# Kernel optimization log

Measured on AMD Instinct MI355X. Metric: run time of the kernel, lower is better.

The kernel has to match this reference:

```python
import jax, jax.numpy as jnp
import numpy as np

DN = ('NCHW', 'OIHW', 'NCHW')

def _conv(x, w, b):
    y = jax.lax.conv_general_dilated(x, w, (2, 2), 'SAME', dimension_numbers=DN)
    return jax.nn.relu(y + b[None, :, None, None])

def setup_inputs() -> dict:
    key = jax.random.key(0)
    ks = jax.random.split(key, 20)
    B, S, V, D, NC = 64, 128, 32000, 512, 1000
    inp = {}
    inp['images'] = jax.random.normal(ks[0], (B, 3, 224, 224), jnp.float32)
    inp['sequences'] = jax.random.randint(ks[1], (B, S), 0, V)
    inp['lengths'] = jax.random.randint(ks[2], (B,), 1, S + 1)
    inp['lengths_var'] = inp['lengths']
    s = 0.02
    inp['emb'] = jax.random.normal(ks[3], (V, D), jnp.float32) * s
    # SimpleCNN(3): 4 strided conv blocks 3->64->128->256->512, final_dim=512
    chans = [3, 64, 128, 256, 512]
    for i in range(4):
        inp[f'cw{i+1}'] = jax.random.normal(ks[4 + i], (chans[i + 1], chans[i], 3, 3), jnp.float32) * s
        inp[f'cb{i+1}'] = jnp.zeros((chans[i + 1],), jnp.float32)
    inp['rnn_w'] = jax.random.normal(ks[8], (D, D), jnp.float32) * s
    inp['rnn_b'] = jnp.zeros((D,), jnp.float32)
    inp['fc1_w'] = jax.random.normal(ks[9], (D + 512, 512), jnp.float32) * s
    inp['fc1_b'] = jnp.zeros((512,), jnp.float32)
    inp['fc2_w'] = jax.random.normal(ks[10], (512, 512), jnp.float32) * s
    inp['fc2_b'] = jnp.zeros((512,), jnp.float32)
    inp['clf_w'] = jax.random.normal(ks[11], (512, NC), jnp.float32) * s
    inp['clf_b'] = jnp.zeros((NC,), jnp.float32)
    return inp

def reference(images, sequences, lengths, lengths_var, emb, cw1, cb1, cw2, cb2, cw3, cb3, cw4, cb4, rnn_w, rnn_b, fc1_w, fc1_b, fc2_w, fc2_b, clf_w, clf_b):
    B, S = sequences.shape
    # masked mean over valid tokens (replaces the per-sample python loop)
    we = emb[sequences]                                   # [B,S,512]
    mask = (jnp.arange(S)[None, :] < lengths[:, None]).astype(we.dtype)
    batch_means = (we * mask[:, :, None]).sum(1) / lengths.astype(we.dtype)[:, None]
    sent = batch_means @ rnn_w + rnn_b                    # [B,512]
    # SimpleCNN + global avg pool -> [B,512,1,1] -> squeeze
    x = _conv(images, cw1, cb1)
    x = _conv(x, cw2, cb2)
    x = _conv(x, cw3, cb3)
    x = _conv(x, cw4, cb4)
    img = x.mean(axis=(2, 3))                             # [B,512]
    feats = jnp.concatenate([img, sent], axis=1)          # [B,1024]
    h = jax.nn.relu(feats @ fc1_w + fc1_b)
    h = jax.nn.relu(h @ fc2_w + fc2_b)                    # dropout = identity (eval)
    return h @ clf_w + clf_b
```

## Files before the change

### kernel.cpp

```cpp
#include <hip/hip_runtime.h>
#include <hip/hip_bf16.h>
#include <cstddef>
#include <cstdint>

typedef unsigned short u16;
typedef __attribute__((ext_vector_type(8))) short bf16x8;
typedef __attribute__((ext_vector_type(4))) float f32x4;
typedef __attribute__((ext_vector_type(8))) unsigned short u16x8;

static __device__ __forceinline__ u16 f2bf(float x) {
  unsigned u = __float_as_uint(x);
  u += 0x7fffu + ((u >> 16) & 1u);
  return (u16)(u >> 16);
}
static __device__ __forceinline__ float bflo(unsigned u) { return __uint_as_float(u << 16); }
static __device__ __forceinline__ float bfhi(unsigned u) { return __uint_as_float(u & 0xffff0000u); }

static __device__ __forceinline__ void gll16(const u16* g, u16* l) {
  __builtin_amdgcn_global_load_lds(
      (const __attribute__((address_space(1))) void*)g,
      (__attribute__((address_space(3))) void*)l, 16, 0, 0);
}

static __device__ __forceinline__ int xcd_swizzle(int orig, int nwg) {
  const int q = nwg >> 3, r = nwg & 7;
  const int xcd = orig & 7, idx = orig >> 3;
  return (xcd < r ? xcd * (q + 1) : r * (q + 1) + (xcd - r) * q) + idx;
}

static __device__ __forceinline__ void halo_store(u16* buf, int H, int W, int C,
                                                  long long i) {
  const int c8n = C >> 3;
  const int c8 = (int)(i % c8n);
  long long rem = i / c8n;
  const int p = (int)(rem % (W + 1 + H));
  const int n = (int)(rem / (W + 1 + H));
  int y, x;
  if (p <= W) { y = H; x = p; } else { y = p - (W + 1); x = W; }
  const u16x8 z = {0, 0, 0, 0, 0, 0, 0, 0};
  *(u16x8*)(buf + (((size_t)n * (H + 1) + y) * (W + 1) + x) * C + c8 * 8) = z;
}
__global__ __launch_bounds__(256) void zero_halo3(u16* __restrict__ A,
                                                  u16* __restrict__ B,
                                                  u16* __restrict__ Cb, int nimg) {
  long long i = (long long)blockIdx.x * 256 + threadIdx.x;
  const long long cA = (long long)nimg * 225 * 8;
  const long long cB = (long long)nimg * 113 * 16;
  const long long cC = (long long)nimg * 57 * 32;
  if (i < cA) { halo_store(A, 112, 112, 64, i); return; }
  i -= cA;
  if (i < cB) { halo_store(B, 56, 56, 128, i); return; }
  i -= cB;
  if (i < cC) halo_store(Cb, 28, 28, 256, i);
}

__global__ __launch_bounds__(256) void conv1_s2(
    const float* __restrict__ in,
    const float* __restrict__ w,
    const float* __restrict__ bias,
    u16* __restrict__ out) {
  __shared__ float sw[64 * 27];
  __shared__ float sb[64];
  __shared__ u16 so[256 * 64];
  const int tid = threadIdx.x;
  if (tid < 64) sb[tid] = bias[tid];
  for (int i = tid; i < 64 * 27; i += 256) sw[i] = w[i];
  __syncthreads();
  const int n = blockIdx.y;
  const int by = blockIdx.x / 7, bx = blockIdx.x % 7;
  const int oy = by * 16 + (tid >> 4), ox = bx * 16 + (tid & 15);
  const bool colv = (ox != 111);
  const float* ib = in + (size_t)n * 3 * 224 * 224 + (size_t)(2 * oy) * 224 + 2 * ox;

  float v[27];
  #pragma unroll
  for (int c = 0; c < 3; ++c)
    #pragma unroll
    for (int r = 0; r < 3; ++r) {
      const bool rowv = !(oy == 111 && r == 2);
      const float* rp = ib + (size_t)c * 50176 + r * 224;
      float2 p = {0.f, 0.f};
      float x2 = 0.f;
      if (rowv) {
        p = *(const float2*)rp;
        if (colv) x2 = rp[2];
      }
      v[c * 9 + r * 3 + 0] = p.x;
      v[c * 9 + r * 3 + 1] = p.y;
      v[c * 9 + r * 3 + 2] = x2;
    }

  #pragma unroll
  for (int kc = 0; kc < 8; ++kc) {
    u16x8 pack;
    #pragma unroll
    for (int k8 = 0; k8 < 8; ++k8) {
      const int k = kc * 8 + k8;
      float a = sb[k];
      const float* wk = &sw[k * 27];
      #pragma unroll
      for (int t = 0; t < 27; ++t) a = fmaf(v[t], wk[t], a);
      pack[k8] = f2bf(fmaxf(a, 0.f));
    }
    *(u16x8*)&so[(tid * 8 + (kc ^ (tid & 7))) * 8] = pack;
  }
  __syncthreads();
  u16* obase = out + (((size_t)n * 113 + by * 16) * 113 + bx * 16) * 64;
  #pragma unroll
  for (int it = 0; it < 8; ++it) {
    const int row = it * 2 + (tid >> 7);
    const int q = tid & 127;
    const int px = q >> 3, c8 = q & 7;
    const int p = row * 16 + px;
    u16x8 v8 = *(const u16x8*)&so[(p * 8 + (c8 ^ (p & 7))) * 8];
    *(u16x8*)(obase + ((size_t)row * 113 + px) * 64 + c8 * 8) = v8;
  }
}

static __device__ __forceinline__ void pack_one(const float* __restrict__ w,
                                                u16* __restrict__ pw,
                                                int CB, int NB, int C, int idx) {
  const int j = idx & 7;
  const int L = (idx >> 3) & 63;
  int t = idx >> 9;
  const int nbg = t % NB; t /= NB;
  const int cb = t % CB;
  const int tap = t / CB;
  const int n = nbg * 16 + (L & 15);
  const int c = cb * 32 + ((L >> 4) << 3) + j;
  pw[idx] = f2bf(w[((size_t)n * C + c) * 9 + tap]);
}
__global__ __launch_bounds__(256) void pack_all(
    const float* __restrict__ w2, const float* __restrict__ w3,
    const float* __restrict__ w4, u16* __restrict__ p2,
    u16* __restrict__ p3, u16* __restrict__ p4) {
  int i = blockIdx.x * 256 + threadIdx.x;
  if (i < 9 * 64 * 128) { pack_one(w2, p2, 2, 8, 64, i); return; }
  i -= 9 * 64 * 128;
  if (i < 9 * 128 * 256) { pack_one(w3, p3, 4, 16, 128, i); return; }
  i -= 9 * 128 * 256;
  if (i < 9 * 256 * 512) pack_one(w4, p4, 8, 32, 256, i);
}

template<int C, int K, int OH, int OW>
__global__ __launch_bounds__(256, 3) void conv3x3s2_mfma(
    const u16* __restrict__ in,
    const u16* __restrict__ pw,
    const float* __restrict__ bias,
    u16* __restrict__ out,
    int M_total) {
  constexpr int IH = 2 * OH, IW = 2 * OW;
  constexpr int PIW = IW + 1;
  constexpr int P = OH * OW;
  constexpr int CB = C / 32, NB = K / 16;
  constexpr int STEPS = 9 * CB;
  static_assert(STEPS % 3 == 0, "triple-buffer rotation needs STEPS%3==0");

  __shared__ u16 lds[3][8192];

  const int bm = xcd_swizzle(blockIdx.x, gridDim.x);
  const int nbh = blockIdx.y;
  const int lane = threadIdx.x & 63, wv = threadIdx.x >> 6;
  const int mh = wv >> 1, nh = wv & 1;

  int s_aoff[4];
  #pragma unroll
  for (int mf = 0; mf < 4; ++mf) {
    int pm = bm * 128 + mh * 64 + mf * 16 + (lane & 15);
    if (pm >= M_total) pm = M_total - 1;
    const int n = pm / P;
    const int p = pm - n * P;
    const int oy = p / OW, ox = p - oy * OW;
    s_aoff[mf] = ((n * (IH + 1) + 2 * oy) * PIW + 2 * ox) * C + ((lane >> 4) << 3);
  }

  f32x4 acc[4][4];
  #pragma unroll
  for (int mf = 0; mf < 4; ++mf)
    #pragma unroll
    for (int nf = 0; nf < 4; ++nf) acc[mf][nf] = (f32x4){0.f, 0.f, 0.f, 0.f};

  auto STAGE = [&](int st, int buf) {
    if (nh == 0) {
      const int cb = st & (CB - 1);
      const int tap = st / CB;
      const int r = tap / 3, s = tap - 3 * r;
      const int toff = (r * PIW + s) * C + cb * 32;
      #pragma unroll
      for (int mf = 0; mf < 4; ++mf)
        gll16(in + s_aoff[mf] + toff, &lds[buf][(mh * 4 + mf) * 512]);
    } else {
      const u16* bp = pw + ((size_t)st * NB + nbh * 8 + mh * 4) * 512 + lane * 8;
      #pragma unroll
      for (int nf = 0; nf < 4; ++nf)
        gll16(bp + nf * 512, &lds[buf][4096 + (mh * 4 + nf) * 512]);
    }
  };
  auto COMPUTE = [&](int buf) {
    bf16x8 a[4], b[4];
    #pragma unroll
    for (int mf = 0; mf < 4; ++mf)
      a[mf] = *(const bf16x8*)&lds[buf][(mh * 4 + mf) * 512 + lane * 8];
    #pragma unroll
    for (int nf = 0; nf < 4; ++nf)
      b[nf] = *(const bf16x8*)&lds[buf][4096 + (nh * 4 + nf) * 512 + lane * 8];
    #pragma unroll
    for (int mf = 0; mf < 4; ++mf)
      #pragma unroll
      for (int nf = 0; nf < 4; ++nf)
        acc[mf][nf] = __builtin_amdgcn_mfma_f32_16x16x32_bf16(a[mf], b[nf], acc[mf][nf], 0, 0, 0);
  };
  auto PHASE = [&](int s, int bufC, int bufS) {
    const bool more = (s + 2) < STEPS;
    if (more) STAGE(s + 2, bufS);
    __builtin_amdgcn_s_setprio(1);
    COMPUTE(bufC);
    __builtin_amdgcn_s_setprio(0);
    if (more) asm volatile("s_waitcnt vmcnt(4)" ::: "memory");
    else      asm volatile("s_waitcnt vmcnt(0)" ::: "memory");
    __builtin_amdgcn_s_barrier();
    __builtin_amdgcn_sched_barrier(0);
  };

  STAGE(0, 0);
  STAGE(1, 1);
  asm volatile("s_waitcnt vmcnt(4)" ::: "memory");
  __builtin_amdgcn_s_barrier();
  __builtin_amdgcn_sched_barrier(0);

  for (int st = 0; st < STEPS; st += 3) {
    PHASE(st + 0, 0, 2);
    PHASE(st + 1, 1, 0);
    PHASE(st + 2, 2, 1);
  }

  const int rowg = (lane >> 4) << 2;
  #pragma unroll
  for (int mf = 0; mf < 4; ++mf)
    #pragma unroll
    for (int nf = 0; nf < 4; ++nf) {
      const int ch = (nbh * 8 + nh * 4 + nf) * 16 + (lane & 15);
      const float bv = bias[ch];
      #pragma unroll
      for (int rr = 0; rr < 4; ++rr) {
        const int pm = bm * 128 + mh * 64 + mf * 16 + rowg + rr;
        if (pm < M_total) {
          const int n = pm / P;
          const int p = pm - n * P;
          const int oy = p / OW, ox = p - oy * OW;
          out[(((size_t)n * (OH + 1) + oy) * (OW + 1) + ox) * K + ch] =
              f2bf(fmaxf(acc[mf][nf][rr] + bv, 0.f));
        }
      }
    }
}

__global__ __launch_bounds__(256) void avgpool_nhwc(
    const u16* __restrict__ in, float* __restrict__ feats, int n0) {
  const int n = blockIdx.x, t = threadIdx.x;
  const u16* p = in + (size_t)n * (15 * 15 * 512) + t * 2;
  float s0 = 0.f, s1 = 0.f;
  for (int y = 0; y < 14; ++y)
    #pragma unroll
    for (int x = 0; x < 14; ++x) {
      unsigned u = *(const unsigned*)(p + (size_t)(y * 15 + x) * 512);
      s0 += bflo(u);
      s1 += bfhi(u);
    }
  float* f = feats + (size_t)(n0 + n) * 1024;
  f[2 * t] = s0 * (1.f / 196.f);
  f[2 * t + 1] = s1 * (1.f / 196.f);
}

__global__ __launch_bounds__(256) void embed_mean_kernel(
    const int* __restrict__ seq, const int* __restrict__ len,
    const float* __restrict__ emb, float* __restrict__ means) {
  __shared__ float part[3][512];
  const int b = blockIdx.x;
  const int L = len[b];
  const int sg = threadIdx.x >> 6;
  const int d0 = (threadIdx.x & 63) * 8;
  float a[8] = {0.f, 0.f, 0.f, 0.f, 0.f, 0.f, 0.f, 0.f};
  for (int s = sg; s < L; s += 4) {
    const float* e = emb + (size_t)seq[b * 128 + s] * 512 + d0;
    float4 v0 = *(const float4*)e, v1 = *(const float4*)(e + 4);
    a[0] += v0.x; a[1] += v0.y; a[2] += v0.z; a[3] += v0.w;
    a[4] += v1.x; a[5] += v1.y; a[6] += v1.z; a[7] += v1.w;
  }
  if (sg) {
    #pragma unroll
    for (int j = 0; j < 8; ++j) part[sg - 1][d0 + j] = a[j];
  }
  __syncthreads();
  if (sg == 0) {
    const float inv = 1.f / (float)L;
    #pragma unroll
    for (int j = 0; j < 8; ++j)
      means[(size_t)b * 512 + d0 + j] =
          (a[j] + part[0][d0 + j] + part[1][d0 + j] + part[2][d0 + j]) * inv;
  }
}

template<int K, int N, bool RELU>
__global__ __launch_bounds__(256) void fc_kernel(
    const float* __restrict__ x, int ldx,
    const float* __restrict__ w, const float* __restrict__ bias,
    float* __restrict__ out, int ldo) {
  __shared__ float row[2][K];
  const int m0 = blockIdx.y * 2;
  for (int i = threadIdx.x; i < 2 * K; i += 256)
    row[i / K][i % K] = x[(size_t)(m0 + i / K) * ldx + (i % K)];
  __syncthreads();
  const int col = blockIdx.x * 256 + threadIdx.x;
  if (col < N) {
    float acc[2][4] = {{0.f, 0.f, 0.f, 0.f}, {0.f, 0.f, 0.f, 0.f}};
    for (int k = 0; k < K; k += 4) {
      float w0 = w[(size_t)(k + 0) * N + col];
      float w1 = w[(size_t)(k + 1) * N + col];
      float w2 = w[(size_t)(k + 2) * N + col];
      float w3 = w[(size_t)(k + 3) * N + col];
      #pragma unroll
      for (int m = 0; m < 2; ++m) {
        acc[m][0] = fmaf(row[m][k + 0], w0, acc[m][0]);
        acc[m][1] = fmaf(row[m][k + 1], w1, acc[m][1]);
        acc[m][2] = fmaf(row[m][k + 2], w2, acc[m][2]);
        acc[m][3] = fmaf(row[m][k + 3], w3, acc[m][3]);
      }
    }
    const float bv = bias[col];
    #pragma unroll
    for (int m = 0; m < 2; ++m) {
      float a = acc[m][0] + acc[m][1] + acc[m][2] + acc[m][3] + bv;
      out[(size_t)(m0 + m) * ldo + col] = RELU ? fmaxf(a, 0.f) : a;
    }
  }
}

extern "C" void kernel_launch(void* const* d_in, const int* in_sizes, int n_in,
                              void* d_out, int out_size, void* d_ws, size_t ws_size,
                              hipStream_t stream) {
  const float* images = (const float*)d_in[0];
  const int*   seq    = (const int*)d_in[1];
  const int*   len    = (const int*)d_in[2];
  const float* emb    = (const float*)d_in[4];
  const float* cw1 = (const float*)d_in[5];  const float* cb1 = (const float*)d_in[6];
  const float* cw2 = (const float*)d_in[7];  const float* cb2 = (const float*)d_in[8];
  const float* cw3 = (const float*)d_in[9];  const float* cb3 = (const float*)d_in[10];
  const float* cw4 = (const float*)d_in[11]; const float* cb4 = (const float*)d_in[12];
  const float* rnn_w = (const float*)d_in[13]; const float* rnn_b = (const float*)d_in[14];
  const float* fc1_w = (const float*)d_in[15]; const float* fc1_b = (const float*)d_in[16];
  const float* fc2_w = (const float*)d_in[17]; const float* fc2_b = (const float*)d_in[18];
  const float* clf_w = (const float*)d_in[19]; const float* clf_b = (const float*)d_in[20];
  float* out = (float*)d_out;

  const size_t A_E = (size_t)113 * 113 * 64;
  const size_t B_E = (size_t)57 * 57 * 128;
  const size_t C_E = (size_t)29 * 29 * 256;
  const size_t D_E = (size_t)15 * 15 * 512;
  const size_t PW2_E = 9 * 64 * 128, PW3_E = 9 * 128 * 256, PW4_E = 9 * 256 * 512;
  const size_t PER_IMG = (A_E + B_E + C_E + D_E) * 2;
  const size_t FIXED = (PW2_E + PW3_E + PW4_E) * 2 +
                       (size_t)(64 * 512 + 64 * 1024 + 64 * 512 + 64 * 512) * 4;
  int chunk = 64;
  if (ws_size < FIXED + 64 * PER_IMG) {
    size_t avail = (ws_size > FIXED) ? (ws_size - FIXED) : 0;
    size_t c = avail / PER_IMG;
    chunk = (c < 1) ? 1 : (c > 64 ? 64 : (int)c);
  }
  u16* bufA = (u16*)d_ws;
  u16* bufB = bufA + (size_t)chunk * A_E;
  u16* bufC = bufB + (size_t)chunk * B_E;
  u16* bufD = bufC + (size_t)chunk * C_E;
  u16* pw2 = bufD + (size_t)chunk * D_E;
  u16* pw3 = pw2 + PW2_E;
  u16* pw4 = pw3 + PW3_E;
  float* means = (float*)(pw4 + PW4_E);
  float* feats = means + 64 * 512;
  float* h1 = feats + 64 * 1024;
  float* h2 = h1 + 64 * 512;

  {
    const int pk_total = 9 * 64 * 128 + 9 * 128 * 256 + 9 * 256 * 512;
    pack_all<<<(pk_total + 255) / 256, 256, 0, stream>>>(cw2, cw3, cw4, pw2, pw3, pw4);
    long long zt = (long long)chunk * (225 * 8 + 113 * 16 + 57 * 32);
    zero_halo3<<<(int)((zt + 255) / 256), 256, 0, stream>>>(bufA, bufB, bufC, chunk);
  }

  embed_mean_kernel<<<64, 256, 0, stream>>>(seq, len, emb, means);
  fc_kernel<512, 512, false><<<dim3(2, 32), 256, 0, stream>>>(
      means, 512, rnn_w, rnn_b, feats + 512, 1024);

  for (int n0 = 0; n0 < 64; n0 += chunk) {
    int nb = 64 - n0; if (nb > chunk) nb = chunk;
    conv1_s2<<<dim3(49, nb), 256, 0, stream>>>(
        images + (size_t)n0 * 3 * 224 * 224, cw1, cb1, bufA);
    const int M2 = nb * 56 * 56, M3 = nb * 28 * 28, M4 = nb * 14 * 14;
    conv3x3s2_mfma<64, 128, 56, 56><<<dim3((M2 + 127) / 128, 1), 256, 0, stream>>>(
        bufA, pw2, cb2, bufB, M2);
    conv3x3s2_mfma<128, 256, 28, 28><<<dim3((M3 + 127) / 128, 2), 256, 0, stream>>>(
        bufB, pw3, cb3, bufC, M3);
    conv3x3s2_mfma<256, 512, 14, 14><<<dim3((M4 + 127) / 128, 4), 256, 0, stream>>>(
        bufC, pw4, cb4, bufD, M4);
    avgpool_nhwc<<<nb, 256, 0, stream>>>(bufD, feats, n0);
  }

  fc_kernel<1024, 512, true ><<<dim3(2, 32), 256, 0, stream>>>(feats, 1024, fc1_w, fc1_b, h1, 512);
  fc_kernel<512,  512, true ><<<dim3(2, 32), 256, 0, stream>>>(h1,    512,  fc2_w, fc2_b, h2, 512);
  fc_kernel<512, 1000, false><<<dim3(4, 32), 256, 0, stream>>>(h2,    512,  clf_w, clf_b, out, 1000);
}
```

Baseline: 376.0 us.

## Store intermediate activations in column-parity-folded layout for strided conv gathers

```diff
diff --git a/kernel.cpp b/kernel.cpp
--- a/kernel.cpp
+++ b/kernel.cpp
@@ -28,30 +28,37 @@
   return (xcd < r ? xcd * (q + 1) : r * (q + 1) + (xcd - r) * q) + idx;
 }
 
-static __device__ __forceinline__ void halo_store(u16* buf, int H, int W, int C,
-                                                  long long i) {
+
+static __device__ __forceinline__ void halo_store_f(u16* buf, int IH, int PC,
+                                                    int C, long long i) {
   const int c8n = C >> 3;
   const int c8 = (int)(i % c8n);
   long long rem = i / c8n;
-  const int p = (int)(rem % (W + 1 + H));
-  const int n = (int)(rem / (W + 1 + H));
-  int y, x;
-  if (p <= W) { y = H; x = p; } else { y = p - (W + 1); x = W; }
+  const int per = 2 * PC + 2 * IH;
+  const int p = (int)(rem % per);
+  const int n = (int)(rem / per);
+  size_t row_off;
+  if (p < 2 * PC) {
+    row_off = ((size_t)(n * (IH + 1) + IH) * 2 * PC) + p;
+  } else {
+    const int q = p - 2 * PC;
+    row_off = ((size_t)(n * (IH + 1) + (q >> 1)) * 2 * PC) + (q & 1) * PC + (PC - 1);
+  }
   const u16x8 z = {0, 0, 0, 0, 0, 0, 0, 0};
-  *(u16x8*)(buf + (((size_t)n * (H + 1) + y) * (W + 1) + x) * C + c8 * 8) = z;
+  *(u16x8*)(buf + row_off * C + c8 * 8) = z;
 }
 __global__ __launch_bounds__(256) void zero_halo3(u16* __restrict__ A,
                                                   u16* __restrict__ B,
                                                   u16* __restrict__ Cb, int nimg) {
   long long i = (long long)blockIdx.x * 256 + threadIdx.x;
-  const long long cA = (long long)nimg * 225 * 8;
-  const long long cB = (long long)nimg * 113 * 16;
-  const long long cC = (long long)nimg * 57 * 32;
-  if (i < cA) { halo_store(A, 112, 112, 64, i); return; }
+  const long long cA = (long long)nimg * 8 * (2 * 57 + 2 * 112);
+  const long long cB = (long long)nimg * 16 * (2 * 29 + 2 * 56);
+  const long long cC = (long long)nimg * 32 * (2 * 15 + 2 * 28);
+  if (i < cA) { halo_store_f(A, 112, 57, 64, i); return; }
   i -= cA;
-  if (i < cB) { halo_store(B, 56, 56, 128, i); return; }
+  if (i < cB) { halo_store_f(B, 56, 29, 128, i); return; }
   i -= cB;
-  if (i < cC) halo_store(Cb, 28, 28, 256, i);
+  if (i < cC) halo_store_f(Cb, 28, 15, 256, i);
 }
 
 __global__ __launch_bounds__(256) void conv1_s2(
@@ -105,7 +112,6 @@
     *(u16x8*)&so[(tid * 8 + (kc ^ (tid & 7))) * 8] = pack;
   }
   __syncthreads();
-  u16* obase = out + (((size_t)n * 113 + by * 16) * 113 + bx * 16) * 64;
   #pragma unroll
   for (int it = 0; it < 8; ++it) {
     const int row = it * 2 + (tid >> 7);
@@ -113,7 +119,9 @@
     const int px = q >> 3, c8 = q & 7;
     const int p = row * 16 + px;
     u16x8 v8 = *(const u16x8*)&so[(p * 8 + (c8 ^ (p & 7))) * 8];
-    *(u16x8*)(obase + ((size_t)row * 113 + px) * 64 + c8 * 8) = v8;
+    const size_t ro = ((size_t)(n * 113 + by * 16 + row) * 2 + (px & 1)) * 57
+                      + bx * 8 + (px >> 1);
+    *(u16x8*)(out + ro * 64 + c8 * 8) = v8;
   }
 }
 
@@ -142,19 +150,21 @@
   if (i < 9 * 256 * 512) pack_one(w4, p4, 8, 32, 256, i);
 }
 
-template<int C, int K, int OH, int OW>
+template<int C, int K, int OH, int OW, bool OUT_FOLD>
 __global__ __launch_bounds__(256, 3) void conv3x3s2_mfma(
     const u16* __restrict__ in,
     const u16* __restrict__ pw,
     const float* __restrict__ bias,
     u16* __restrict__ out,
     int M_total) {
-  constexpr int IH = 2 * OH, IW = 2 * OW;
-  constexpr int PIW = IW + 1;
+  constexpr int IH = 2 * OH;
+  constexpr int IPC = OW + 1;
+  constexpr int IROW = 2 * IPC;
   constexpr int P = OH * OW;
   constexpr int CB = C / 32, NB = K / 16;
   constexpr int STEPS = 9 * CB;
   static_assert(STEPS % 3 == 0, "triple-buffer rotation needs STEPS%3==0");
+  constexpr int OPC = OW / 2 + 1;
 
   __shared__ u16 lds[3][8192];
 
@@ -171,7 +181,7 @@
     const int n = pm / P;
     const int p = pm - n * P;
     const int oy = p / OW, ox = p - oy * OW;
-    s_aoff[mf] = ((n * (IH + 1) + 2 * oy) * PIW + 2 * ox) * C + ((lane >> 4) << 3);
+    s_aoff[mf] = ((n * (IH + 1) + 2 * oy) * IROW + ox) * C + ((lane >> 4) << 3);
   }
 
   f32x4 acc[4][4];
@@ -185,7 +195,7 @@
       const int cb = st & (CB - 1);
       const int tap = st / CB;
       const int r = tap / 3, s = tap - 3 * r;
-      const int toff = (r * PIW + s) * C + cb * 32;
+      const int toff = (r * IROW + (s & 1) * IPC + (s >> 1)) * C + cb * 32;
       #pragma unroll
       for (int mf = 0; mf < 4; ++mf)
         gll16(in + s_aoff[mf] + toff, &lds[buf][(mh * 4 + mf) * 512]);
@@ -248,8 +258,12 @@
           const int n = pm / P;
           const int p = pm - n * P;
           const int oy = p / OW, ox = p - oy * OW;
-          out[(((size_t)n * (OH + 1) + oy) * (OW + 1) + ox) * K + ch] =
-              f2bf(fmaxf(acc[mf][nf][rr] + bv, 0.f));
+          size_t ro;
+          if (OUT_FOLD)
+            ro = ((size_t)(n * (OH + 1) + oy) * 2 + (ox & 1)) * OPC + (ox >> 1);
+          else
+            ro = (size_t)(n * (OH + 1) + oy) * (OW + 1) + ox;
+          out[ro * K + ch] = f2bf(fmaxf(acc[mf][nf][rr] + bv, 0.f));
         }
       }
     }
@@ -353,9 +367,9 @@
   const float* clf_w = (const float*)d_in[19]; const float* clf_b = (const float*)d_in[20];
   float* out = (float*)d_out;
 
-  const size_t A_E = (size_t)113 * 113 * 64;
-  const size_t B_E = (size_t)57 * 57 * 128;
-  const size_t C_E = (size_t)29 * 29 * 256;
+  const size_t A_E = (size_t)113 * 2 * 57 * 64;
+  const size_t B_E = (size_t)57 * 2 * 29 * 128;
+  const size_t C_E = (size_t)29 * 2 * 15 * 256;
   const size_t D_E = (size_t)15 * 15 * 512;
   const size_t PW2_E = 9 * 64 * 128, PW3_E = 9 * 128 * 256, PW4_E = 9 * 256 * 512;
   const size_t PER_IMG = (A_E + B_E + C_E + D_E) * 2;
@@ -382,7 +396,8 @@
   {
     const int pk_total = 9 * 64 * 128 + 9 * 128 * 256 + 9 * 256 * 512;
     pack_all<<<(pk_total + 255) / 256, 256, 0, stream>>>(cw2, cw3, cw4, pw2, pw3, pw4);
-    long long zt = (long long)chunk * (225 * 8 + 113 * 16 + 57 * 32);
+    long long zt = (long long)chunk *
+        (8 * (2 * 57 + 2 * 112) + 16 * (2 * 29 + 2 * 56) + 32 * (2 * 15 + 2 * 28));
     zero_halo3<<<(int)((zt + 255) / 256), 256, 0, stream>>>(bufA, bufB, bufC, chunk);
   }
 
@@ -395,11 +410,11 @@
     conv1_s2<<<dim3(49, nb), 256, 0, stream>>>(
         images + (size_t)n0 * 3 * 224 * 224, cw1, cb1, bufA);
     const int M2 = nb * 56 * 56, M3 = nb * 28 * 28, M4 = nb * 14 * 14;
-    conv3x3s2_mfma<64, 128, 56, 56><<<dim3((M2 + 127) / 128, 1), 256, 0, stream>>>(
+    conv3x3s2_mfma<64, 128, 56, 56, true><<<dim3((M2 + 127) / 128, 1), 256, 0, stream>>>(
         bufA, pw2, cb2, bufB, M2);
-    conv3x3s2_mfma<128, 256, 28, 28><<<dim3((M3 + 127) / 128, 2), 256, 0, stream>>>(
+    conv3x3s2_mfma<128, 256, 28, 28, true><<<dim3((M3 + 127) / 128, 2), 256, 0, stream>>>(
         bufB, pw3, cb3, bufC, M3);
-    conv3x3s2_mfma<256, 512, 14, 14><<<dim3((M4 + 127) / 128, 4), 256, 0, stream>>>(
+    conv3x3s2_mfma<256, 512, 14, 14, false><<<dim3((M4 + 127) / 128, 4), 256, 0, stream>>>(
         bufC, pw4, cb4, bufD, M4);
     avgpool_nhwc<<<nb, 256, 0, stream>>>(bufD, feats, n0);
   }
```

Measured after the change: 381.5 us. No clear change (+1.5%).
